# Kernel tuning notes

Measured on AMD Instinct MI355X. Metric: run time of the kernel, lower is better.

Reference implementation:

```python
import jax, jax.numpy as jnp
import numpy as np

B, C, W = 32, 128, 4096          # batch, channel (= emb_dim = D), window/input_dim
HID = [2048, 1024, 512]          # encoder hidden dims (last dim transforms)
K, D = 512, 128                  # codebook: K = hidden_dims[-1], D = emb_dim
BETA = 0.25


def setup_inputs() -> dict:
    key = jax.random.key(0)
    ks = jax.random.split(key, 12)
    def lin(k, fan_in, fan_out):
        return jax.random.normal(k, (fan_in, fan_out), jnp.float32) * (1.0 / np.sqrt(fan_in))
    inp = {"x": jax.random.normal(ks[0], (B, C, W), jnp.float32)}
    edims = [W] + HID  # 4096 -> 2048 -> 1024 -> 512
    for i in range(3):
        inp[f"ew{i}"] = lin(ks[1 + i], edims[i], edims[i + 1])
        inp[f"eb{i}"] = jnp.zeros((edims[i + 1],), jnp.float32)
    inp["codebook"] = jax.random.uniform(ks[4], (K, D), jnp.float32, -1.0 / K, 1.0 / K)
    ddims = [512, 1024, 2048, 4096]  # decoder mirrors encoder
    for i in range(3):
        inp[f"dw{i}"] = lin(ks[5 + i], ddims[i], ddims[i + 1])
        inp[f"db{i}"] = jnp.zeros((ddims[i + 1],), jnp.float32)
    return inp


def reference(x, ew0, eb0, ew1, eb1, ew2, eb2, codebook, dw0, db0, dw1, db1, dw2, db2):
    # ---- encoder: LinearBlock = Linear + ReLU over last dim ----
    h = x
    for wgt, b in ((ew0, eb0), (ew1, eb1), (ew2, eb2)):
        h = jax.nn.relu(h @ wgt + b)            # [B, C, L] with L shrinking to 512

    # ---- VectorQuantizer1d ----
    lat = jnp.swapaxes(h, 1, 2)                 # [B, L, D]
    flat = lat.reshape(-1, D)                   # [B*L, D]
    # cdist^2 via expansion, then argmin -> nearest-codebook lookup
    dist = (jnp.sum(flat * flat, axis=1, keepdims=True)
            + jnp.sum(codebook * codebook, axis=1)
            - 2.0 * flat @ codebook.T)          # [B*L, K]
    inds = jnp.argmin(dist, axis=1)             # [B*L]
    q = codebook[inds].reshape(lat.shape)       # one-hot matmul == gather

    commit = jnp.mean((jax.lax.stop_gradient(q) - lat) ** 2)
    embed = jnp.mean((q - jax.lax.stop_gradient(lat)) ** 2)
    vq_loss = BETA * commit + embed

    q_st = lat + jax.lax.stop_gradient(q - lat)  # straight-through estimator
    z = jnp.swapaxes(q_st, 1, 2)                 # back to [B, D, L]

    # ---- decoder: Linear+ReLU blocks, last block has no activation ----
    for i, (wgt, b) in enumerate(((dw0, db0), (dw1, db1), (dw2, db2))):
        z = z @ wgt + b
        if i < 2:
            z = jax.nn.relu(z)
    return z, x, vq_loss
```

## Files before the change

### kernel.cpp

```cpp
#include <hip/hip_runtime.h>


typedef _Float16 f16;
typedef _Float16 f16x8 __attribute__((ext_vector_type(8)));
typedef _Float16 f16x4 __attribute__((ext_vector_type(4)));
typedef float    f32x4 __attribute__((ext_vector_type(4)));

typedef const unsigned int __attribute__((address_space(1)))* gp1_t;
typedef unsigned int __attribute__((address_space(3)))*       lp3_t;

__device__ __forceinline__ void gl_lds16(const void* g, void* l) {
  __builtin_amdgcn_global_load_lds((gp1_t)g, (lp3_t)l, 16, 0, 0);
}

#define BATCH 32
#define CDIM  128
#define WDIM  4096
#define LDIM  512
#define KCB   512
#define DCB   128

#define SX    128.0f
#define SW    256.0f
#define SA    256.0f
#define SCB   4096.0f
#define SQ    4096.0f


#define G8_SRC(t, As, Bs, kk) \
  const f16 *As, *Bs; int kk; \
  { int ts_ = (t) < NTloc ? (t) : NTloc - 1; int kg_ = (t0 + ts_) << 6; \
    if (SPLIT) { int sg_ = (kg_ >= 2 * K) ? 2 : ((kg_ >= K) ? 1 : 0); \
      kk = kg_ - sg_ * K; As = (sg_ == 2) ? Al : Ah; Bs = (sg_ == 1) ? Bl : Bh; } \
    else { As = Ah; Bs = Bh; kk = kg_; } }

#define G8_STAGE(src, row0, kk, off) \
  _Pragma("unroll") \
  for (int j_ = 0; j_ < 2; ++j_) { \
    const int p_ = j_ * 8192 + tid * 16; \
    const int r_ = p_ >> 7; \
    const int c_ = (p_ >> 4) & 7; \
    gl_lds16((src) + (size_t)((row0) + r_) * K + (kk) + ((c_ ^ (r_ & 7)) << 3), \
             smem + (off) + p_); \
  }

#define G8_STAGE_A(t, u) do { G8_SRC(t, As_, Bs_, kk_) \
  G8_STAGE(As_, m0 + (u) * 128, kk_, ((t) & 1) * ASZ + (u) * 16384) } while (0)
#define G8_STAGE_B(t, u) do { G8_SRC(t, As_, Bs_, kk_) \
  G8_STAGE(Bs_, n0 + (u) * 128, kk_, BBASE + ((t) & 1) * BSZ + (u) * 16384) } while (0)

#define G8_READ_A(buf, mh) \
  _Pragma("unroll") \
  for (int m_ = 0; m_ < MR2; ++m_) { \
    const int r_ = wr * (MR * 16) + ((mh) * MR2 + m_) * 16 + fr; \
    _Pragma("unroll") \
    for (int ks_ = 0; ks_ < 2; ++ks_) \
      ar[m_][ks_] = *(const f16x8*)(smem + (buf) * ASZ + r_ * 128 + \
                                    ((((ks_ << 2) + hq) ^ (r_ & 7)) << 4)); \
  }

#define G8_READ_B(buf, nh, br) \
  _Pragma("unroll") \
  for (int n_ = 0; n_ < 2; ++n_) { \
    const int r_ = wc * 64 + ((nh) * 2 + n_) * 16 + fr; \
    _Pragma("unroll") \
    for (int ks_ = 0; ks_ < 2; ++ks_) \
      br[n_][ks_] = *(const f16x8*)(smem + BBASE + (buf) * BSZ + r_ * 128 + \
                                    ((((ks_ << 2) + hq) ^ (r_ & 7)) << 4)); \
  }

#define G8_MFMA(mh, nh, br) \
  _Pragma("unroll") \
  for (int m_ = 0; m_ < MR2; ++m_) \
  _Pragma("unroll") \
  for (int n_ = 0; n_ < 2; ++n_) \
  _Pragma("unroll") \
  for (int ks_ = 0; ks_ < 2; ++ks_) \
    acc[(mh) * MR2 + m_][(nh) * 2 + n_] = __builtin_amdgcn_mfma_f32_16x16x32_f16( \
        ar[m_][ks_], br[n_][ks_], acc[(mh) * MR2 + m_][(nh) * 2 + n_], 0, 0, 0);

#define G8_BAR() do { asm volatile("" ::: "memory"); \
  __builtin_amdgcn_s_barrier(); asm volatile("" ::: "memory"); } while (0)
#define G8_LGKM0() do { asm volatile("s_waitcnt lgkmcnt(0)" ::: "memory"); \
  __builtin_amdgcn_sched_barrier(0); } while (0)
#define G8_VMGATE() do { \
  if constexpr (BUNITS == 2) asm volatile("s_waitcnt vmcnt(4)" ::: "memory"); \
  else                       asm volatile("s_waitcnt vmcnt(2)" ::: "memory"); } while (0)
#define G8_PRIO1() __builtin_amdgcn_s_setprio(1)
#define G8_PRIO0() __builtin_amdgcn_s_setprio(0)

template<int SPLIT, int EPI, int WM, int WN, int MR>
__global__ __launch_bounds__(512, 2)
void vq_gemm8(const f16* __restrict__ Ah, const f16* __restrict__ Al,
              const f16* __restrict__ Bh, const f16* __restrict__ Bl,
              const float* __restrict__ bias,
              void* __restrict__ Co, void* __restrict__ Co2,
              int M, int N, int K, int NTloc, float unscale, float outscale)
{
  constexpr int MR2 = MR / 2;
  constexpr int GBM = WM * MR * 16;
  constexpr int GBN = WN * 64;
  constexpr int BUNITS = GBN / 128;
  constexpr int ASZ = GBM * 128;
  constexpr int BSZ = GBN * 128;
  constexpr int BBASE = 2 * ASZ;
  constexpr int LDSZ = 2 * ASZ + 2 * BSZ;

  __shared__ __align__(16) char smem[LDSZ];

  const int tid = threadIdx.x;
  const int lane = tid & 63;
  const int w = tid >> 6;
  const int wr = w / WN, wc = w % WN;
  const int fr = lane & 15, hq = lane >> 4;

  const int nbx = N / GBN;
  const int cpx = (int)gridDim.x >> 3;
  const int swz = ((int)blockIdx.x & 7) * cpx + ((int)blockIdx.x >> 3);
  const int bx = swz % nbx, by = swz / nbx;
  const int m0 = by * GBM, n0 = bx * GBN;
  const int t0 = (int)blockIdx.y * NTloc;

  const int NI = NTloc >> 1;

  f32x4 acc[MR][4] = {};
  f16x8 ar[MR2][2], br0[2][2], br1[2][2];

  G8_STAGE_B(0, 0); if constexpr (BUNITS == 2) G8_STAGE_B(0, 1);
  G8_STAGE_A(0, 0); G8_STAGE_A(0, 1);
  G8_STAGE_B(1, 0); if constexpr (BUNITS == 2) G8_STAGE_B(1, 1);

  for (int i = 0; i < NI; ++i) {
    const int to = 2 * i + 1, te = 2 * i + 2, to2 = 2 * i + 3;
    if constexpr (BUNITS == 1) {
      G8_VMGATE(); G8_BAR();
      G8_READ_A(0, 0) G8_READ_B(0, 0, br0) G8_READ_B(0, 1, br1)
      G8_STAGE_A(to, 0); G8_STAGE_A(to, 1);
      G8_BAR(); G8_LGKM0();
      G8_PRIO1(); G8_MFMA(0, 0, br0) G8_MFMA(0, 1, br1) G8_PRIO0();
      G8_BAR();
      G8_READ_A(0, 1)
      G8_STAGE_B(te, 0);
      G8_BAR(); G8_LGKM0();
      G8_PRIO1(); G8_MFMA(1, 0, br0) G8_MFMA(1, 1, br1) G8_PRIO0();
      G8_VMGATE(); G8_BAR();
      G8_READ_A(1, 0) G8_READ_B(1, 0, br0) G8_READ_B(1, 1, br1)
      G8_STAGE_A(te, 0); G8_STAGE_A(te, 1);
      G8_BAR(); G8_LGKM0();
      G8_PRIO1(); G8_MFMA(0, 0, br0) G8_MFMA(0, 1, br1) G8_PRIO0();
      G8_BAR();
      G8_READ_A(1, 1)
      G8_STAGE_B(to2, 0);
      G8_BAR(); G8_LGKM0();
      G8_PRIO1(); G8_MFMA(1, 0, br0) G8_MFMA(1, 1, br1) G8_PRIO0();
    } else {
      G8_VMGATE(); G8_BAR();
      G8_READ_A(0, 0) G8_READ_B(0, 0, br0)
      G8_STAGE_A(to, 0);
      G8_BAR(); G8_LGKM0(); G8_PRIO1(); G8_MFMA(0, 0, br0) G8_PRIO0();
      G8_BAR();
      G8_READ_B(0, 1, br1)
      G8_STAGE_A(to, 1);
      G8_BAR(); G8_LGKM0(); G8_PRIO1(); G8_MFMA(0, 1, br1) G8_PRIO0();
      G8_BAR();
      G8_READ_A(0, 1)
      G8_STAGE_B(te, 0);
      G8_BAR(); G8_LGKM0(); G8_PRIO1(); G8_MFMA(1, 0, br0) G8_PRIO0();
      G8_BAR();
      G8_STAGE_B(te, 1);
      G8_BAR(); G8_PRIO1(); G8_MFMA(1, 1, br1) G8_PRIO0();
      G8_VMGATE(); G8_BAR();
      G8_READ_A(1, 0) G8_READ_B(1, 0, br0)
      G8_STAGE_A(te, 0);
      G8_BAR(); G8_LGKM0(); G8_PRIO1(); G8_MFMA(0, 0, br0) G8_PRIO0();
      G8_BAR();
      G8_READ_B(1, 1, br1)
      G8_STAGE_A(te, 1);
      G8_BAR(); G8_LGKM0(); G8_PRIO1(); G8_MFMA(0, 1, br1) G8_PRIO0();
      G8_BAR();
      G8_READ_A(1, 1)
      G8_STAGE_B(to2, 0);
      G8_BAR(); G8_LGKM0(); G8_PRIO1(); G8_MFMA(1, 0, br0) G8_PRIO0();
      G8_BAR();
      G8_STAGE_B(to2, 1);
      G8_BAR(); G8_PRIO1(); G8_MFMA(1, 1, br1) G8_PRIO0();
    }
  }

  float* Pslab = (EPI == 4) ? ((float*)Co + (size_t)blockIdx.y * M * N) : nullptr;
  const int r4 = hq * 4;
#pragma unroll
  for (int mi = 0; mi < MR; ++mi) {
#pragma unroll
    for (int ni = 0; ni < 4; ++ni) {
      const int col = n0 + wc * 64 + ni * 16 + fr;
      const float bv = (EPI == 0 || EPI == 4) ? 0.f : bias[col];
#pragma unroll
      for (int j = 0; j < 4; ++j) {
        const int row = m0 + wr * (MR * 16) + mi * 16 + r4 + j;
        const size_t idx = (size_t)row * N + col;
        float y = acc[mi][ni][j] * unscale;
        if (EPI == 4) { Pslab[idx] = y; continue; }
        if (EPI != 0) y += bv;
        if (EPI == 1 || EPI == 2) y = fmaxf(y, 0.f);
        if (EPI == 0 || EPI == 3) ((float*)Co)[idx] = y;
        else {
          const float ys = y * outscale;
          const f16 hv = (f16)ys;
          ((f16*)Co)[idx] = hv;
          if (EPI == 1) ((f16*)Co2)[idx] = (f16)(ys - (float)hv);
        }
      }
    }
  }
}

template<int NS>
__global__ void vq_ksum(const float* __restrict__ P, const float* __restrict__ bias,
                        f16* __restrict__ Oh, f16* __restrict__ Ol,
                        int MN, int N, float unscale, float outscale)
{
  const int i4 = (blockIdx.x * 256 + threadIdx.x) * 4;
  if (i4 >= MN) return;
  float4 s = ((const float4*)P)[i4 >> 2];
#pragma unroll
  for (int sl = 1; sl < NS; ++sl) {
    const float4 v = ((const float4*)(P + (size_t)sl * MN))[i4 >> 2];
    s.x += v.x; s.y += v.y; s.z += v.z; s.w += v.w;
  }
  const int col = i4 % N;
  f16x4 h, l;
#pragma unroll
  for (int j = 0; j < 4; ++j) {
    float y = (&s.x)[j] * unscale + bias[col + j];
    y = fmaxf(y, 0.f) * outscale;
    const f16 hv = (f16)y;
    h[j] = hv;
    l[j] = (f16)(y - (float)hv);
  }
  *(f16x4*)&Oh[i4] = h;
  *(f16x4*)&Ol[i4] = l;
}

#define BM 128
#define BN 128
#define BK 32

template<int SPLIT, int EPI>
__global__ __launch_bounds__(256, 2)
void vq_gemm(const f16* __restrict__ Ah, const f16* __restrict__ Al,
             const f16* __restrict__ Bh, const f16* __restrict__ Bl,
             const float* __restrict__ bias,
             void* __restrict__ Co, void* __restrict__ Co2,
             int M, int N, int K, float unscale, float outscale)
{
  __shared__ __align__(16) f16 sAh[BM * BK];
  __shared__ __align__(16) f16 sBh[BN * BK];
  __shared__ __align__(16) f16 sAl[SPLIT ? BM * BK : 8];
  __shared__ __align__(16) f16 sBl[SPLIT ? BN * BK : 8];

  const int tid  = threadIdx.x;
  const int lane = tid & 63;
  const int w    = tid >> 6;
  const int nb   = N / BN;
  const int bx   = blockIdx.x % nb;
  const int by   = blockIdx.x / nb;
  const int m0   = by * BM, n0 = bx * BN;
  const int wr   = w >> 1, wc = w & 1;
  const int fr   = lane & 15;
  const int ko   = (lane >> 4) * 8;

  f32x4 acc[4][4] = {};

  const int srow = lane >> 2;
  const int skb  = (lane & 3) * 8;

  for (int k0 = 0; k0 < K; k0 += BK) {
#pragma unroll
    for (int i = 0; i < 2; ++i) {
      const int c  = w * 2 + i;
      const size_t ga = (size_t)(m0 + c * 16 + srow) * K + k0 + skb;
      const size_t gb = (size_t)(n0 + c * 16 + srow) * K + k0 + skb;
      gl_lds16(Ah + ga, &sAh[c * 512]);
      gl_lds16(Bh + gb, &sBh[c * 512]);
      if (SPLIT) {
        gl_lds16(Al + ga, &sAl[c * 512]);
        gl_lds16(Bl + gb, &sBl[c * 512]);
      }
    }
    __syncthreads();

    f16x8 ah[4], bh[4], al[4], bl[4];
#pragma unroll
    for (int mi = 0; mi < 4; ++mi) {
      const int r = (wr * 64 + mi * 16 + fr) * BK + ko;
      ah[mi] = *(const f16x8*)&sAh[r];
      if (SPLIT) al[mi] = *(const f16x8*)&sAl[r];
    }
#pragma unroll
    for (int ni = 0; ni < 4; ++ni) {
      const int r = (wc * 64 + ni * 16 + fr) * BK + ko;
      bh[ni] = *(const f16x8*)&sBh[r];
      if (SPLIT) bl[ni] = *(const f16x8*)&sBl[r];
    }
#pragma unroll
    for (int mi = 0; mi < 4; ++mi)
#pragma unroll
      for (int ni = 0; ni < 4; ++ni) {
        acc[mi][ni] = __builtin_amdgcn_mfma_f32_16x16x32_f16(ah[mi], bh[ni], acc[mi][ni], 0, 0, 0);
        if (SPLIT) {
          acc[mi][ni] = __builtin_amdgcn_mfma_f32_16x16x32_f16(ah[mi], bl[ni], acc[mi][ni], 0, 0, 0);
          acc[mi][ni] = __builtin_amdgcn_mfma_f32_16x16x32_f16(al[mi], bh[ni], acc[mi][ni], 0, 0, 0);
        }
      }
    __syncthreads();
  }

  const int r4 = (lane >> 4) * 4;
#pragma unroll
  for (int mi = 0; mi < 4; ++mi) {
#pragma unroll
    for (int ni = 0; ni < 4; ++ni) {
      const int col = n0 + wc * 64 + ni * 16 + fr;
      const float bv = (EPI == 0) ? 0.0f : bias[col];
#pragma unroll
      for (int j = 0; j < 4; ++j) {
        const int row = m0 + wr * 64 + mi * 16 + r4 + j;
        float y = acc[mi][ni][j] * unscale;
        if (EPI != 0) y += bv;
        if (EPI == 1 || EPI == 2) y = fmaxf(y, 0.0f);
        const size_t idx = (size_t)row * N + col;
        if (EPI == 0 || EPI == 3) {
          ((float*)Co)[idx] = y;
        } else {
          const float ys = y * outscale;
          const f16 hv = (f16)ys;
          ((f16*)Co)[idx] = hv;
          if (EPI == 1) ((f16*)Co2)[idx] = (f16)(ys - (float)hv);
        }
      }
    }
  }
}

__global__ void vq_split(const float* __restrict__ in, f16* __restrict__ hi,
                         f16* __restrict__ lo, int n4, float scale,
                         float* __restrict__ raw)
{
  const int i = blockIdx.x * 256 + threadIdx.x;
  if (i >= n4) return;
  const float4 v = ((const float4*)in)[i];
  if (raw) ((float4*)raw)[i] = v;
  f16x4 h, l;
#pragma unroll
  for (int j = 0; j < 4; ++j) {
    const float s = (&v.x)[j] * scale;
    const f16 hh = (f16)s;
    h[j] = hh;
    l[j] = (f16)(s - (float)hh);
  }
  *(f16x4*)&hi[i * 4] = h;
  *(f16x4*)&lo[i * 4] = l;
}

template<int WRITE_LO>
__global__ void vq_tsplit(const float* __restrict__ W, f16* __restrict__ Th,
                          f16* __restrict__ Tl, int K, int N, float scale)
{
  __shared__ float t[32][33];
  const int n0 = blockIdx.x * 32, k0 = blockIdx.y * 32;
  const int tx = threadIdx.x & 31, ty = threadIdx.x >> 5;
#pragma unroll
  for (int i = 0; i < 4; ++i)
    t[ty + i * 8][tx] = W[(size_t)(k0 + ty + i * 8) * N + n0 + tx];
  __syncthreads();
#pragma unroll
  for (int i = 0; i < 4; ++i) {
    const int n = n0 + ty + i * 8;
    const float v = t[tx][ty + i * 8] * scale;
    const f16 hv = (f16)v;
    Th[(size_t)n * K + k0 + tx] = hv;
    if (WRITE_LO) Tl[(size_t)n * K + k0 + tx] = (f16)(v - (float)hv);
  }
}

__global__ void vq_tpose(const f16* __restrict__ Hh, const f16* __restrict__ Hl,
                         f16* __restrict__ Fh, f16* __restrict__ Fl)
{
  __shared__ f16 th[32][33];
  __shared__ f16 tl[32][33];
  const int bidx = blockIdx.x;
  const int b = bidx >> 6, rem = bidx & 63;
  const int l0 = (rem >> 2) * 32, c0 = (rem & 3) * 32;
  const int tx = threadIdx.x & 31, ty = threadIdx.x >> 5;
  const size_t hbase = (size_t)b * CDIM * LDIM;
#pragma unroll
  for (int i = 0; i < 4; ++i) {
    const int c = c0 + ty + i * 8;
    th[ty + i * 8][tx] = Hh[hbase + (size_t)c * LDIM + l0 + tx];
    tl[ty + i * 8][tx] = Hl[hbase + (size_t)c * LDIM + l0 + tx];
  }
  __syncthreads();
  const size_t fbase = (size_t)b * LDIM * DCB;
#pragma unroll
  for (int i = 0; i < 4; ++i) {
    const int l = l0 + ty + i * 8;
    Fh[fbase + (size_t)l * DCB + c0 + tx] = th[tx][ty + i * 8];
    Fl[fbase + (size_t)l * DCB + c0 + tx] = tl[tx][ty + i * 8];
  }
}

__global__ void vq_cbnorm(const float* __restrict__ cb, float* __restrict__ cbn)
{
  const int k = blockIdx.x * 256 + threadIdx.x;
  if (k >= KCB) return;
  float s = 0.f;
  for (int c = 0; c < DCB; ++c) { const float v = cb[k * DCB + c]; s += v * v; }
  cbn[k] = s;
}

__global__ void vq_argmin(const float* __restrict__ G, const float* __restrict__ cbn,
                          int* __restrict__ inds)
{
  const int row = blockIdx.x;
  const int lane = threadIdx.x;
  const float* g = G + (size_t)row * KCB;
  float best = 1e30f; int bi = 0;
#pragma unroll
  for (int j = 0; j < 8; ++j) {
    const int k = j * 64 + lane;
    const float d = cbn[k] - 2.0f * g[k];
    if (d < best) { best = d; bi = k; }
  }
  for (int off = 32; off; off >>= 1) {
    const float ov = __shfl_xor(best, off);
    const int oi = __shfl_xor(bi, off);
    if (ov < best || (ov == best && oi < bi)) { best = ov; bi = oi; }
  }
  if (lane == 0) inds[row] = bi;
}

__global__ void vq_gather(const float* __restrict__ cb, const int* __restrict__ inds,
                          f16* __restrict__ z0)
{
  const int t = blockIdx.x * 256 + threadIdx.x;
  const int l = t & 511, c = (t >> 9) & 127, b = t >> 16;
  const int ind = inds[b * LDIM + l];
  z0[t] = (f16)(cb[ind * DCB + c] * SQ);
}

__global__ void vq_loss(const f16* __restrict__ Fh, const f16* __restrict__ Fl,
                        const float* __restrict__ cb, const int* __restrict__ inds,
                        float* __restrict__ partials)
{
  const int gw = (blockIdx.x * 256 + threadIdx.x) >> 6;
  const int lane = threadIdx.x & 63;
  float s = 0.f;
  for (int r = gw; r < BATCH * LDIM; r += 1024) {
    const int ind = inds[r];
    const f16* fh = Fh + (size_t)r * DCB;
    const f16* fl = Fl + (size_t)r * DCB;
    const float* q = cb + (size_t)ind * DCB;
#pragma unroll
    for (int j = 0; j < 2; ++j) {
      const int c = j * 64 + lane;
      const float lat = ((float)fh[c] + (float)fl[c]) * (1.0f / SA);
      const float d = q[c] - lat;
      s += d * d;
    }
  }
  for (int off = 32; off; off >>= 1) s += __shfl_xor(s, off);
  __shared__ float wsum[4];
  if (lane == 0) wsum[threadIdx.x >> 6] = s;
  __syncthreads();
  if (threadIdx.x == 0) partials[blockIdx.x] = wsum[0] + wsum[1] + wsum[2] + wsum[3];
}

__global__ void vq_loss_final(const float* __restrict__ partials, float* __restrict__ out)
{
  float s = partials[threadIdx.x];
  for (int off = 32; off; off >>= 1) s += __shfl_xor(s, off);
  __shared__ float wsum[4];
  if ((threadIdx.x & 63) == 0) wsum[threadIdx.x >> 6] = s;
  __syncthreads();
  if (threadIdx.x == 0)
    out[0] = (wsum[0] + wsum[1] + wsum[2] + wsum[3]) * (1.25f / (float)(BATCH * LDIM * DCB));
}

extern "C" void kernel_launch(void* const* d_in, const int* in_sizes, int n_in,
                              void* d_out, int out_size, void* d_ws, size_t ws_size,
                              hipStream_t stream)
{
  const float* x   = (const float*)d_in[0];
  const float* ew0 = (const float*)d_in[1];
  const float* eb0 = (const float*)d_in[2];
  const float* ew1 = (const float*)d_in[3];
  const float* eb1 = (const float*)d_in[4];
  const float* ew2 = (const float*)d_in[5];
  const float* eb2 = (const float*)d_in[6];
  const float* cb  = (const float*)d_in[7];
  const float* dw0 = (const float*)d_in[8];
  const float* db0 = (const float*)d_in[9];
  const float* dw1 = (const float*)d_in[10];
  const float* db1 = (const float*)d_in[11];
  const float* dw2 = (const float*)d_in[12];
  const float* db2 = (const float*)d_in[13];
  float* out = (float*)d_out;

  constexpr size_t N_X  = 4096ull * 4096;
  constexpr size_t N_E0 = 4096ull * 2048, N_E1 = 2048ull * 1024, N_E2 = 1024ull * 512;
  constexpr size_t N_CB = 512ull * 128;
  constexpr size_t N_D0 = 512ull * 1024, N_D1 = 1024ull * 2048, N_D2 = 2048ull * 4096;
  constexpr size_t N_H0 = 4096ull * 2048, N_H1 = 4096ull * 1024, N_H2 = 4096ull * 512;
  constexpr size_t N_FL = 16384ull * 128;
  constexpr size_t N_Z1 = 4096ull * 1024;

  constexpr size_t O_EW0H = 0;
  constexpr size_t O_EW0L = O_EW0H + N_E0 * 2;
  constexpr size_t O_EW1H = O_EW0L + N_E0 * 2;
  constexpr size_t O_EW1L = O_EW1H + N_E1 * 2;
  constexpr size_t O_EW2H = O_EW1L + N_E1 * 2;
  constexpr size_t O_EW2L = O_EW2H + N_E2 * 2;
  constexpr size_t O_CBH  = O_EW2L + N_E2 * 2;
  constexpr size_t O_CBL  = O_CBH + N_CB * 2;
  constexpr size_t O_DW0  = O_CBL + N_CB * 2;
  constexpr size_t O_DW1  = O_DW0 + N_D0 * 2;
  constexpr size_t O_DW2  = O_DW1 + N_D1 * 2;
  constexpr size_t O_XH   = O_DW2 + N_D2 * 2;
  constexpr size_t O_XL   = O_XH + N_X * 2;
  constexpr size_t O_H0H  = O_XL + N_X * 2;
  constexpr size_t O_H0L  = O_H0H + N_H0 * 2;
  constexpr size_t O_H1H  = O_H0L + N_H0 * 2;
  constexpr size_t O_H1L  = O_H1H + N_H1 * 2;
  constexpr size_t O_H2H  = O_H1L + N_H1 * 2;
  constexpr size_t O_H2L  = O_H2H + N_H2 * 2;
  constexpr size_t O_FLH  = O_H2L + N_H2 * 2;
  constexpr size_t O_FLL  = O_FLH + N_FL * 2;
  constexpr size_t O_G    = O_XH;
  constexpr size_t O_INDS = O_XL;
  constexpr size_t O_CBN  = O_XL + (1ull << 17);
  constexpr size_t O_PART = O_XL + (1ull << 18);
  constexpr size_t O_Z0   = O_XL + (1ull << 20);
  constexpr size_t O_ZH1  = O_Z0 + N_H2 * 2;
  constexpr size_t O_ZH2  = O_ZH1 + N_Z1 * 2;

  char* ws = (char*)d_ws;
  f16*   XH = (f16*)(ws + O_XH);   f16* XL = (f16*)(ws + O_XL);
  f16* EW0H = (f16*)(ws + O_EW0H); f16* EW0L = (f16*)(ws + O_EW0L);
  f16* EW1H = (f16*)(ws + O_EW1H); f16* EW1L = (f16*)(ws + O_EW1L);
  f16* EW2H = (f16*)(ws + O_EW2H); f16* EW2L = (f16*)(ws + O_EW2L);
  f16*  CBH = (f16*)(ws + O_CBH);  f16* CBL = (f16*)(ws + O_CBL);
  f16*  DW0 = (f16*)(ws + O_DW0);  f16* DW1 = (f16*)(ws + O_DW1);  f16* DW2 = (f16*)(ws + O_DW2);
  f16*  H0H = (f16*)(ws + O_H0H);  f16* H0L = (f16*)(ws + O_H0L);
  f16*  H1H = (f16*)(ws + O_H1H);  f16* H1L = (f16*)(ws + O_H1L);
  f16*  H2H = (f16*)(ws + O_H2H);  f16* H2L = (f16*)(ws + O_H2L);
  f16*  FLH = (f16*)(ws + O_FLH);  f16* FLL = (f16*)(ws + O_FLL);
  float*  G = (float*)(ws + O_G);
  int* INDS = (int*)(ws + O_INDS);
  float* CBN = (float*)(ws + O_CBN);
  float* PART = (float*)(ws + O_PART);
  f16*   Z0 = (f16*)(ws + O_Z0);
  f16*  ZH1 = (f16*)(ws + O_ZH1);
  f16*  ZH2 = (f16*)(ws + O_ZH2);
  float* PSL = out;

  vq_split<<<(int)(N_X / 4 / 256), 256, 0, stream>>>(x, XH, XL, (int)(N_X / 4), SX,
                                                     out + 16777216);
  vq_split<<<(int)(N_CB / 4 / 256), 256, 0, stream>>>(cb, CBH, CBL, (int)(N_CB / 4), SCB,
                                                      nullptr);
  vq_tsplit<1><<<dim3(2048 / 32, 4096 / 32), 256, 0, stream>>>(ew0, EW0H, EW0L, 4096, 2048, SW);
  vq_tsplit<1><<<dim3(1024 / 32, 2048 / 32), 256, 0, stream>>>(ew1, EW1H, EW1L, 2048, 1024, SW);
  vq_tsplit<1><<<dim3(512 / 32, 1024 / 32), 256, 0, stream>>>(ew2, EW2H, EW2L, 1024, 512, SW);
  vq_tsplit<0><<<dim3(1024 / 32, 512 / 32), 256, 0, stream>>>(dw0, DW0, nullptr, 512, 1024, SW);
  vq_tsplit<0><<<dim3(2048 / 32, 1024 / 32), 256, 0, stream>>>(dw1, DW1, nullptr, 1024, 2048, SW);
  vq_tsplit<0><<<dim3(4096 / 32, 2048 / 32), 256, 0, stream>>>(dw2, DW2, nullptr, 2048, 4096, SW);

  vq_gemm8<1, 4, 2, 4, 8><<<dim3(128, 2), 512, 0, stream>>>(
      XH, XL, EW0H, EW0L, nullptr, PSL, nullptr, 4096, 2048, 4096, 96, 1.0f, 0.f);
  vq_ksum<2><<<(int)(N_H0 / 4 / 256), 256, 0, stream>>>(
      PSL, eb0, H0H, H0L, (int)N_H0, 2048, 1.0f / (SX * SW), SA);
  vq_gemm8<1, 4, 2, 4, 8><<<dim3(64, 4), 512, 0, stream>>>(
      H0H, H0L, EW1H, EW1L, nullptr, PSL, nullptr, 4096, 1024, 2048, 24, 1.0f, 0.f);
  vq_ksum<4><<<(int)(N_H1 / 4 / 256), 256, 0, stream>>>(
      PSL, eb1, H1H, H1L, (int)N_H1, 1024, 1.0f / (SA * SW), SA);
  vq_gemm<1, 1><<<(4096 / BM) * (512 / BN), 256, 0, stream>>>(
      H1H, H1L, EW2H, EW2L, eb2, H2H, H2L, 4096, 512, 1024, 1.0f / (SA * SW), SA);

  vq_tpose<<<BATCH * 64, 256, 0, stream>>>(H2H, H2L, FLH, FLL);
  vq_gemm<1, 0><<<(16384 / BM) * (512 / BN), 256, 0, stream>>>(
      FLH, FLL, CBH, CBL, nullptr, G, nullptr, 16384, 512, 128, 1.0f / (SA * SCB), 0.f);
  vq_cbnorm<<<2, 256, 0, stream>>>(cb, CBN);
  vq_argmin<<<16384, 64, 0, stream>>>(G, CBN, INDS);
  vq_gather<<<(BATCH * CDIM * LDIM) / 256, 256, 0, stream>>>(cb, INDS, Z0);
  vq_loss<<<256, 256, 0, stream>>>(FLH, FLL, cb, INDS, PART);
  vq_loss_final<<<1, 256, 0, stream>>>(PART, out + 33554432);

  vq_gemm<0, 2><<<(4096 / BM) * (1024 / BN), 256, 0, stream>>>(
      Z0, nullptr, DW0, nullptr, db0, ZH1, nullptr, 4096, 1024, 512, 1.0f / (SQ * SW), SQ);
  vq_gemm8<0, 2, 4, 2, 4><<<dim3(256, 1), 512, 0, stream>>>(
      ZH1, nullptr, DW1, nullptr, db1, ZH2, nullptr, 4096, 2048, 1024, 16, 1.0f / (SQ * SW), SQ);
  vq_gemm8<0, 3, 2, 4, 8><<<dim3(256, 1), 512, 0, stream>>>(
      ZH2, nullptr, DW2, nullptr, db2, out, nullptr, 4096, 4096, 2048, 32, 1.0f / (SQ * SW), 0.f);

  (void)in_sizes; (void)n_in; (void)out_size; (void)ws_size;
}
```

Baseline: 540.7 us.

## Add split-precision GEMM kernel sharing A/B tiles across hi/lo products for encoder

Adds a new split-K GEMM kernel for the first two encoder layers. It stages the hi and lo halves of both A and B for each 32-wide K step together in LDS and reuses each loaded tile for three MFMA products (hh, hl, lh). The old kernel treated the three split terms as separate K segments, tripling the K range, so each A and B tile had to be reloaded. This cuts global and LDS traffic per FLOP, at the cost of a larger 128 KB LDS footprint, a deeper vmcnt-gated pipeline, and higher register pressure from the 256x256 tile.

```diff
diff --git a/kernel.cpp b/kernel.cpp
--- a/kernel.cpp
+++ b/kernel.cpp
@@ -26,6 +26,124 @@
 #define SCB   4096.0f
 #define SQ    4096.0f
 
+#define G8_BAR() do { asm volatile("" ::: "memory"); \
+  __builtin_amdgcn_s_barrier(); asm volatile("" ::: "memory"); } while (0)
+#define G8_LGKM0() do { asm volatile("s_waitcnt lgkmcnt(0)" ::: "memory"); \
+  __builtin_amdgcn_sched_barrier(0); } while (0)
+#define G8_PRIO1() __builtin_amdgcn_s_setprio(1)
+#define G8_PRIO0() __builtin_amdgcn_s_setprio(0)
+
+
+#define GS_STAGE(src, row0, kk, off) \
+  _Pragma("unroll") \
+  for (int j_ = 0; j_ < 2; ++j_) { \
+    const int p_ = j_ * 8192 + tid * 16; \
+    const int r_ = p_ >> 6; \
+    const int c_ = (p_ >> 4) & 3; \
+    gl_lds16((src) + (size_t)((row0) + r_) * K + (kk) + ((c_ ^ ((r_ >> 1) & 3)) << 3), \
+             smem + (off) + p_); \
+  }
+
+#define GS_ST(tt, pb, SRC, row0, poff) do { \
+  const int tc_ = (tt) < NTloc ? (tt) : NTloc - 1; \
+  const int kk_ = (t0 + tc_) << 5; \
+  GS_STAGE(SRC, row0, kk_, (pb) * 65536 + (poff)) } while (0)
+
+#define GS_READ_A(pb, HL, half, dst) \
+  _Pragma("unroll") \
+  for (int m_ = 0; m_ < 4; ++m_) { \
+    const int r_ = wr * 128 + ((half) * 4 + m_) * 16 + fr; \
+    dst[m_] = *(const f16x8*)(smem + (pb) * 65536 + (HL) * 16384 + r_ * 64 + swz16); \
+  }
+
+#define GS_READ_B(pb, HL, brr) \
+  _Pragma("unroll") \
+  for (int n_ = 0; n_ < 4; ++n_) { \
+    const int r_ = wc * 64 + n_ * 16 + fr; \
+    brr[n_] = *(const f16x8*)(smem + (pb) * 65536 + 32768 + (HL) * 16384 + r_ * 64 + swz16); \
+  }
+
+#define GS_MFMA(aarr, half, brr) \
+  _Pragma("unroll") \
+  for (int m_ = 0; m_ < 4; ++m_) \
+  _Pragma("unroll") \
+  for (int n_ = 0; n_ < 4; ++n_) \
+    acc[(half) * 4 + m_][n_] = __builtin_amdgcn_mfma_f32_16x16x32_f16( \
+        aarr[m_], brr[n_], acc[(half) * 4 + m_][n_], 0, 0, 0);
+
+__global__ __launch_bounds__(512, 2)
+void vq_gemmS(const f16* __restrict__ Ah, const f16* __restrict__ Al,
+              const f16* __restrict__ Bh, const f16* __restrict__ Bl,
+              float* __restrict__ Co, int M, int N, int K, int NTloc)
+{
+  __shared__ __align__(16) char smem[131072];
+
+  const int tid = threadIdx.x;
+  const int lane = tid & 63;
+  const int w = tid >> 6;
+  const int wr = w >> 2, wc = w & 3;
+  const int fr = lane & 15, hq = lane >> 4;
+  const int swz16 = (hq ^ ((fr >> 1) & 3)) << 4;
+
+  const int nbx = N / 256;
+  const int cpx = (int)gridDim.x >> 3;
+  const int swzb = ((int)blockIdx.x & 7) * cpx + ((int)blockIdx.x >> 3);
+  const int bx = swzb % nbx, by = swzb / nbx;
+  const int m0 = by * 256, n0 = bx * 256;
+  const int t0 = (int)blockIdx.y * NTloc;
+
+  f32x4 acc[8][4] = {};
+  f16x8 ah0[4], ah1[4], al0[4], al1[4], bh[4], bl[4];
+
+  GS_ST(0, 0, Bh, n0, 32768); GS_ST(0, 0, Bl, n0, 49152);
+  GS_ST(0, 0, Ah, m0, 0);     GS_ST(0, 0, Al, m0, 16384);
+  GS_ST(1, 1, Bh, n0, 32768); GS_ST(1, 1, Bl, n0, 49152);
+  GS_ST(1, 1, Ah, m0, 0);     GS_ST(1, 1, Al, m0, 16384);
+
+  int pb = 0;
+  for (int t = 0; t < NTloc; ++t) {
+    asm volatile("s_waitcnt vmcnt(8)" ::: "memory");
+    G8_BAR();
+    GS_READ_A(pb, 0, 0, ah0) GS_READ_B(pb, 0, bh)
+    G8_BAR(); G8_LGKM0();
+    G8_PRIO1(); GS_MFMA(ah0, 0, bh) G8_PRIO0();
+    G8_BAR();
+    GS_READ_A(pb, 1, 0, al0) GS_READ_B(pb, 1, bl)
+    GS_ST(t + 2, pb, Bh, n0, 32768);
+    G8_BAR(); G8_LGKM0();
+    G8_PRIO1(); GS_MFMA(ah0, 0, bl) G8_PRIO0();
+    G8_BAR();
+    GS_READ_A(pb, 0, 1, ah1)
+    GS_ST(t + 2, pb, Bl, n0, 49152);
+    G8_BAR(); G8_LGKM0();
+    G8_PRIO1(); GS_MFMA(al0, 0, bh) G8_PRIO0();
+    G8_BAR();
+    GS_READ_A(pb, 1, 1, al1)
+    GS_ST(t + 2, pb, Ah, m0, 0);
+    G8_BAR(); G8_LGKM0();
+    G8_PRIO1(); GS_MFMA(ah1, 1, bh) G8_PRIO0();
+    G8_BAR();
+    GS_ST(t + 2, pb, Al, m0, 16384);
+    G8_PRIO1(); GS_MFMA(ah1, 1, bl) GS_MFMA(al1, 1, bh) G8_PRIO0();
+    pb ^= 1;
+  }
+
+  float* Pslab = Co + (size_t)blockIdx.y * M * N;
+  const int r4 = hq * 4;
+#pragma unroll
+  for (int mi = 0; mi < 8; ++mi) {
+#pragma unroll
+    for (int ni = 0; ni < 4; ++ni) {
+      const int col = n0 + wc * 64 + ni * 16 + fr;
+#pragma unroll
+      for (int j = 0; j < 4; ++j) {
+        const int row = m0 + wr * 128 + mi * 16 + r4 + j;
+        Pslab[(size_t)row * N + col] = acc[mi][ni][j];
+      }
+    }
+  }
+}
+
 
 #define G8_SRC(t, As, Bs, kk) \
   const f16 *As, *Bs; int kk; \
@@ -79,15 +197,9 @@
     acc[(mh) * MR2 + m_][(nh) * 2 + n_] = __builtin_amdgcn_mfma_f32_16x16x32_f16( \
         ar[m_][ks_], br[n_][ks_], acc[(mh) * MR2 + m_][(nh) * 2 + n_], 0, 0, 0);
 
-#define G8_BAR() do { asm volatile("" ::: "memory"); \
-  __builtin_amdgcn_s_barrier(); asm volatile("" ::: "memory"); } while (0)
-#define G8_LGKM0() do { asm volatile("s_waitcnt lgkmcnt(0)" ::: "memory"); \
-  __builtin_amdgcn_sched_barrier(0); } while (0)
 #define G8_VMGATE() do { \
   if constexpr (BUNITS == 2) asm volatile("s_waitcnt vmcnt(4)" ::: "memory"); \
   else                       asm volatile("s_waitcnt vmcnt(2)" ::: "memory"); } while (0)
-#define G8_PRIO1() __builtin_amdgcn_s_setprio(1)
-#define G8_PRIO0() __builtin_amdgcn_s_setprio(0)
 
 template<int SPLIT, int EPI, int WM, int WN, int MR>
 __global__ __launch_bounds__(512, 2)
@@ -187,20 +299,18 @@
     }
   }
 
-  float* Pslab = (EPI == 4) ? ((float*)Co + (size_t)blockIdx.y * M * N) : nullptr;
   const int r4 = hq * 4;
 #pragma unroll
   for (int mi = 0; mi < MR; ++mi) {
 #pragma unroll
     for (int ni = 0; ni < 4; ++ni) {
       const int col = n0 + wc * 64 + ni * 16 + fr;
-      const float bv = (EPI == 0 || EPI == 4) ? 0.f : bias[col];
+      const float bv = (EPI == 0) ? 0.f : bias[col];
 #pragma unroll
       for (int j = 0; j < 4; ++j) {
         const int row = m0 + wr * (MR * 16) + mi * 16 + r4 + j;
         const size_t idx = (size_t)row * N + col;
         float y = acc[mi][ni][j] * unscale;
-        if (EPI == 4) { Pslab[idx] = y; continue; }
         if (EPI != 0) y += bv;
         if (EPI == 1 || EPI == 2) y = fmaxf(y, 0.f);
         if (EPI == 0 || EPI == 3) ((float*)Co)[idx] = y;
@@ -575,12 +685,12 @@
   vq_tsplit<0><<<dim3(2048 / 32, 1024 / 32), 256, 0, stream>>>(dw1, DW1, nullptr, 1024, 2048, SW);
   vq_tsplit<0><<<dim3(4096 / 32, 2048 / 32), 256, 0, stream>>>(dw2, DW2, nullptr, 2048, 4096, SW);
 
-  vq_gemm8<1, 4, 2, 4, 8><<<dim3(128, 2), 512, 0, stream>>>(
-      XH, XL, EW0H, EW0L, nullptr, PSL, nullptr, 4096, 2048, 4096, 96, 1.0f, 0.f);
+  vq_gemmS<<<dim3(128, 2), 512, 0, stream>>>(
+      XH, XL, EW0H, EW0L, PSL, 4096, 2048, 4096, 64);
   vq_ksum<2><<<(int)(N_H0 / 4 / 256), 256, 0, stream>>>(
       PSL, eb0, H0H, H0L, (int)N_H0, 2048, 1.0f / (SX * SW), SA);
-  vq_gemm8<1, 4, 2, 4, 8><<<dim3(64, 4), 512, 0, stream>>>(
-      H0H, H0L, EW1H, EW1L, nullptr, PSL, nullptr, 4096, 1024, 2048, 24, 1.0f, 0.f);
+  vq_gemmS<<<dim3(64, 4), 512, 0, stream>>>(
+      H0H, H0L, EW1H, EW1L, PSL, 4096, 1024, 2048, 16);
   vq_ksum<4><<<(int)(N_H1 / 4 / 256), 256, 0, stream>>>(
       PSL, eb1, H1H, H1L, (int)N_H1, 1024, 1.0f / (SA * SW), SA);
   vq_gemm<1, 1><<<(4096 / BM) * (512 / BN), 256, 0, stream>>>(
```

Result: no change. 539.8 us (-0.2%).
